# Optimization experiments

Hardware: AMD Instinct MI355X
Metric: run time of the kernel (lower is better)

## Reference

```python
import jax, jax.numpy as jnp
import numpy as np

D_MODEL = 128
REDUCTION = 4
KSIZE = 3
B = D_MODEL  # required by the original code's groups=B conv shape constraint
L = 4096


def setup_inputs() -> dict:
    key = jax.random.key(0)
    ks = jax.random.split(key, 7)
    d, r, K = D_MODEL, REDUCTION, KSIZE
    return {
        "x": jax.random.normal(ks[0], (B, L, d), dtype=jnp.float32),
        "W1": jax.random.normal(ks[1], (d // r, d), dtype=jnp.float32) * (1.0 / np.sqrt(d)),
        "b1": jax.random.normal(ks[2], (d // r,), dtype=jnp.float32) * 0.01,
        "W2": jax.random.normal(ks[3], (K, d // r), dtype=jnp.float32) * (1.0 / np.sqrt(d // r)),
        "b2": jax.random.normal(ks[4], (K,), dtype=jnp.float32) * 0.01,
        "Wc": jax.random.normal(ks[5], (d, d), dtype=jnp.float32) * (1.0 / np.sqrt(d)),
        "bc": jax.random.normal(ks[6], (d,), dtype=jnp.float32) * 0.01,
    }


def reference(x, W1, b1, W2, b2, Wc, bc):
    # x: [B, L, d] with B == d (required by original groups=B conv)
    Bsz, Lseq, d = x.shape
    K = W2.shape[0]
    pad = (K - 1) // 2
    # kernel generation from global average pool
    m = x.mean(axis=1)                                   # [B, d]
    h = jax.nn.gelu(m @ W1.T + b1, approximate=False)    # [B, d//r]
    w = jax.nn.softmax(h @ W2.T + b2, axis=-1)           # [B, K]; row j is the kernel for channel j
    # depthwise-style cross-correlation: y[b, l, c] = sum_k xp[b, l+k, c] * w[c, k]
    xp = jnp.pad(x, ((0, 0), (pad, pad), (0, 0)))        # [B, L+2*pad, d]
    y = sum(xp[:, k:k + Lseq, :] * w[None, None, :, k] for k in range(K))  # [B, L, d]
    # pointwise conv (kernel_size=1) == per-token linear
    return y @ Wc.T + bc                                 # [B, L, d]
```

## Files before the change

kernel.cpp:

```cpp
#include <hip/hip_runtime.h>
#include <hip/hip_bf16.h>

#define D_MODEL 128
#define SEQ_L   4096
#define BATCH   128
#define TM      128
#define NSEG    8

typedef float f4 __attribute__((ext_vector_type(4)));
typedef float f32x4 __attribute__((ext_vector_type(4)));
typedef short bf16x8 __attribute__((ext_vector_type(8)));

__device__ __forceinline__ unsigned short f2bf(float f) {
    union { float f; unsigned u; } v; v.f = f;
    unsigned r = v.u + 0x7FFFu + ((v.u >> 16) & 1u);
    return (unsigned short)(r >> 16);
}

__global__ __launch_bounds__(256) void kmean(const float* __restrict__ x,
                                             float* __restrict__ part) {
    int seg = blockIdx.x, b = blockIdx.y;
    int t = threadIdx.x;
    int c4 = t & 31, ph = t >> 5;
    const f4* xb = reinterpret_cast<const f4*>(x + (size_t)b * SEQ_L * D_MODEL);
    int l0 = seg * (SEQ_L / NSEG);
    f4 acc = {0.f, 0.f, 0.f, 0.f};
    for (int l = l0 + ph; l < l0 + SEQ_L / NSEG; l += 8)
        acc += xb[l * 32 + c4];
    __shared__ f4 red[256];
    red[t] = acc;
    __syncthreads();
    if (t < 32) {
        f4 s = red[t];
        #pragma unroll
        for (int p = 1; p < 8; ++p) s += red[t + 32 * p];
        reinterpret_cast<f4*>(part + ((size_t)b * NSEG + seg) * D_MODEL)[t] = s;
    }
}

__global__ __launch_bounds__(128) void kweights(const float* __restrict__ part,
                                                const float* __restrict__ W1,
                                                const float* __restrict__ b1,
                                                const float* __restrict__ W2,
                                                const float* __restrict__ b2,
                                                float* __restrict__ w) {
    int c = threadIdx.x;
    f4 mv[32];
    #pragma unroll
    for (int d4 = 0; d4 < 32; ++d4) mv[d4] = (f4){0.f, 0.f, 0.f, 0.f};
    for (int s = 0; s < NSEG; ++s) {
        const f4* ps = reinterpret_cast<const f4*>(part + ((size_t)c * NSEG + s) * D_MODEL);
        #pragma unroll
        for (int d4 = 0; d4 < 32; ++d4) mv[d4] += ps[d4];
    }
    #pragma unroll
    for (int d4 = 0; d4 < 32; ++d4) mv[d4] *= (1.0f / (float)SEQ_L);

    float h[32];
    #pragma unroll
    for (int j = 0; j < 32; ++j) {
        const f4* w1r = reinterpret_cast<const f4*>(W1 + j * 128);
        f4 s4 = {0.f, 0.f, 0.f, 0.f};
        #pragma unroll
        for (int d4 = 0; d4 < 32; ++d4) s4 += mv[d4] * w1r[d4];
        float s = s4[0] + s4[1] + s4[2] + s4[3] + b1[j];
        h[j] = 0.5f * s * (1.0f + erff(s * 0.70710678118654752f));
    }
    float lg[3];
    float mx = -1e30f;
    #pragma unroll
    for (int k = 0; k < 3; ++k) {
        float s = b2[k];
        #pragma unroll
        for (int j = 0; j < 32; ++j) s += h[j] * W2[k * 32 + j];
        lg[k] = s;
        mx = fmaxf(mx, s);
    }
    float e[3], den = 0.f;
    #pragma unroll
    for (int k = 0; k < 3; ++k) { e[k] = __expf(lg[k] - mx); den += e[k]; }
    float inv = 1.0f / den;
    #pragma unroll
    for (int k = 0; k < 3; ++k) w[k * 128 + c] = e[k] * inv;
}

__global__ __launch_bounds__(256) void kcvt(const float* __restrict__ Wc,
                                            unsigned short* __restrict__ wcb) {
    int i = blockIdx.x * 256 + threadIdx.x;
    f4 v = reinterpret_cast<const f4*>(Wc)[i];
    ushort4 o;
    o.x = f2bf(v[0]); o.y = f2bf(v[1]); o.z = f2bf(v[2]); o.w = f2bf(v[3]);
    reinterpret_cast<ushort4*>(wcb)[i] = o;
}

__global__ __launch_bounds__(512, 4) void kconv(const float* __restrict__ x,
                                                const float* __restrict__ w,
                                                const unsigned short* __restrict__ wcb,
                                                const float* __restrict__ bc,
                                                float* __restrict__ out) {
    __shared__ __align__(16) unsigned short y_lds[TM][136];
    __shared__ __align__(16) unsigned short wc_lds[128][136];

    int t = threadIdx.x;
    int b = blockIdx.y;
    int l0 = blockIdx.x * TM;
    const float* xb = x + (size_t)b * SEQ_L * D_MODEL;

    int c4 = t & 31;
    f4 w0 = reinterpret_cast<const f4*>(w)[c4];
    f4 w1 = reinterpret_cast<const f4*>(w + 128)[c4];
    f4 w2 = reinterpret_cast<const f4*>(w + 256)[c4];

    {
        int rg = t >> 5;
        int r0 = rg * 8;
        int lb = l0 + r0;
        f4 prev = (lb > 0) ? reinterpret_cast<const f4*>(xb + (size_t)(lb - 1) * D_MODEL)[c4]
                           : (f4){0.f, 0.f, 0.f, 0.f};
        f4 cur = reinterpret_cast<const f4*>(xb + (size_t)lb * D_MODEL)[c4];
        #pragma unroll
        for (int i = 0; i < 8; ++i) {
            int l = lb + i;
            f4 nxt = (l < SEQ_L - 1)
                         ? reinterpret_cast<const f4*>(xb + (size_t)(l + 1) * D_MODEL)[c4]
                         : (f4){0.f, 0.f, 0.f, 0.f};
            f4 y = prev * w0 + cur * w1 + nxt * w2;
            ushort4 yb;
            yb.x = f2bf(y[0]); yb.y = f2bf(y[1]); yb.z = f2bf(y[2]); yb.w = f2bf(y[3]);
            *reinterpret_cast<ushort4*>(&y_lds[r0 + i][c4 * 4]) = yb;
            prev = cur;
            cur = nxt;
        }
    }

    {
        int row = t >> 4;
        int u16 = t & 15;
        #pragma unroll
        for (int p = 0; p < 4; ++p) {
            int rr = row + p * 32;
            uint4 v = reinterpret_cast<const uint4*>(wcb + (size_t)rr * 128)[u16];
            *reinterpret_cast<uint4*>(&wc_lds[rr][u16 * 8]) = v;
        }
    }
    __syncthreads();

    int lane = t & 63, wid = t >> 6;
    int lrow = wid * 16 + (lane & 15);
    int kb = (lane >> 4) * 8;

    f32x4 acc[8];
    #pragma unroll
    for (int n = 0; n < 8; ++n) acc[n] = (f32x4){0.f, 0.f, 0.f, 0.f};

    #pragma unroll
    for (int kc = 0; kc < 4; ++kc) {
        bf16x8 by = *reinterpret_cast<const bf16x8*>(&y_lds[lrow][kc * 32 + kb]);
        #pragma unroll
        for (int n = 0; n < 8; ++n) {
            bf16x8 awc = *reinterpret_cast<const bf16x8*>(&wc_lds[n * 16 + (lane & 15)][kc * 32 + kb]);
            acc[n] = __builtin_amdgcn_mfma_f32_16x16x32_bf16(awc, by, acc[n], 0, 0, 0);
        }
    }

    int l = l0 + wid * 16 + (lane & 15);
    int cb = (lane >> 4) * 4;
    float* orow = out + ((size_t)b * SEQ_L + l) * D_MODEL;
    #pragma unroll
    for (int n = 0; n < 8; ++n) {
        f4 bcv = *reinterpret_cast<const f4*>(bc + n * 16 + cb);
        f4 v = acc[n] + bcv;
        *reinterpret_cast<f4*>(orow + n * 16 + cb) = v;
    }
}

extern "C" void kernel_launch(void* const* d_in, const int* in_sizes, int n_in,
                              void* d_out, int out_size, void* d_ws, size_t ws_size,
                              hipStream_t stream) {
    const float* x  = (const float*)d_in[0];
    const float* W1 = (const float*)d_in[1];
    const float* b1 = (const float*)d_in[2];
    const float* W2 = (const float*)d_in[3];
    const float* b2 = (const float*)d_in[4];
    const float* Wc = (const float*)d_in[5];
    const float* bc = (const float*)d_in[6];
    float* out = (float*)d_out;

    char* ws = (char*)d_ws;
    float* part = (float*)ws;
    float* w    = (float*)(ws + 524288);
    unsigned short* wcb = (unsigned short*)(ws + 526336);

    kmean<<<dim3(NSEG, BATCH), 256, 0, stream>>>(x, part);
    kweights<<<1, 128, 0, stream>>>(part, W1, b1, W2, b2, w);
    kcvt<<<16, 256, 0, stream>>>(Wc, wcb);
    kconv<<<dim3(SEQ_L / TM, BATCH), 512, 0, stream>>>(x, w, wcb, bc, out);
}
```

Baseline: 264.5 us.

## Keep Wc slice in registers per wave and unroll mean reduction

The conv kernel stops staging the bf16 pointwise weight matrix in LDS. Each wave instead loads its own 16 output-channel rows of Wc into registers and loops over 8 token tiles, reading only the y tile from LDS. This cuts the LDS footprint and the per-MFMA LDS reads for weights, at the cost of more scattered output stores. The mean kernel is widened to 512 threads with four independent accumulators to raise memory-level parallelism.

```diff
diff --git a/kernel.cpp b/kernel.cpp
--- a/kernel.cpp
+++ b/kernel.cpp
@@ -6,6 +6,7 @@
 #define BATCH   128
 #define TM      128
 #define NSEG    8
+#define YPAD    132
 
 typedef float f4 __attribute__((ext_vector_type(4)));
 typedef float f32x4 __attribute__((ext_vector_type(4)));
@@ -17,23 +18,31 @@
     return (unsigned short)(r >> 16);
 }
 
-__global__ __launch_bounds__(256) void kmean(const float* __restrict__ x,
+__global__ __launch_bounds__(512) void kmean(const float* __restrict__ x,
                                              float* __restrict__ part) {
     int seg = blockIdx.x, b = blockIdx.y;
     int t = threadIdx.x;
     int c4 = t & 31, ph = t >> 5;
     const f4* xb = reinterpret_cast<const f4*>(x + (size_t)b * SEQ_L * D_MODEL);
     int l0 = seg * (SEQ_L / NSEG);
-    f4 acc = {0.f, 0.f, 0.f, 0.f};
-    for (int l = l0 + ph; l < l0 + SEQ_L / NSEG; l += 8)
-        acc += xb[l * 32 + c4];
-    __shared__ f4 red[256];
+
+    f4 a0 = {0.f,0.f,0.f,0.f}, a1 = a0, a2 = a0, a3 = a0;
+    #pragma unroll
+    for (int i = 0; i < 32; i += 4) {
+        a0 += xb[(l0 + ph + (i + 0) * 16) * 32 + c4];
+        a1 += xb[(l0 + ph + (i + 1) * 16) * 32 + c4];
+        a2 += xb[(l0 + ph + (i + 2) * 16) * 32 + c4];
+        a3 += xb[(l0 + ph + (i + 3) * 16) * 32 + c4];
+    }
+    f4 acc = (a0 + a1) + (a2 + a3);
+
+    __shared__ f4 red[512];
     red[t] = acc;
     __syncthreads();
     if (t < 32) {
         f4 s = red[t];
         #pragma unroll
-        for (int p = 1; p < 8; ++p) s += red[t + 32 * p];
+        for (int p = 1; p < 16; ++p) s += red[t + 32 * p];
         reinterpret_cast<f4*>(part + ((size_t)b * NSEG + seg) * D_MODEL)[t] = s;
     }
 }
@@ -98,13 +107,22 @@
                                                 const unsigned short* __restrict__ wcb,
                                                 const float* __restrict__ bc,
                                                 float* __restrict__ out) {
-    __shared__ __align__(16) unsigned short y_lds[TM][136];
-    __shared__ __align__(16) unsigned short wc_lds[128][136];
+    __shared__ __align__(16) unsigned short y_lds[TM][YPAD];
 
     int t = threadIdx.x;
     int b = blockIdx.y;
     int l0 = blockIdx.x * TM;
     const float* xb = x + (size_t)b * SEQ_L * D_MODEL;
+
+    int lane = t & 63, wid = t >> 6;
+    int co0 = wid * 16;
+    int arow = co0 + (lane & 15);
+    int kb = (lane >> 4) * 8;
+
+    bf16x8 awc[4];
+    #pragma unroll
+    for (int kc = 0; kc < 4; ++kc)
+        awc[kc] = *reinterpret_cast<const bf16x8*>(wcb + (size_t)arow * 128 + kc * 32 + kb);
 
     int c4 = t & 31;
     f4 w0 = reinterpret_cast<const f4*>(w)[c4];
@@ -132,45 +150,28 @@
             cur = nxt;
         }
     }
-
-    {
-        int row = t >> 4;
-        int u16 = t & 15;
-        #pragma unroll
-        for (int p = 0; p < 4; ++p) {
-            int rr = row + p * 32;
-            uint4 v = reinterpret_cast<const uint4*>(wcb + (size_t)rr * 128)[u16];
-            *reinterpret_cast<uint4*>(&wc_lds[rr][u16 * 8]) = v;
-        }
-    }
     __syncthreads();
-
-    int lane = t & 63, wid = t >> 6;
-    int lrow = wid * 16 + (lane & 15);
-    int kb = (lane >> 4) * 8;
 
     f32x4 acc[8];
     #pragma unroll
-    for (int n = 0; n < 8; ++n) acc[n] = (f32x4){0.f, 0.f, 0.f, 0.f};
+    for (int tt = 0; tt < 8; ++tt) acc[tt] = (f32x4){0.f, 0.f, 0.f, 0.f};
 
     #pragma unroll
-    for (int kc = 0; kc < 4; ++kc) {
-        bf16x8 by = *reinterpret_cast<const bf16x8*>(&y_lds[lrow][kc * 32 + kb]);
+    for (int tt = 0; tt < 8; ++tt) {
         #pragma unroll
-        for (int n = 0; n < 8; ++n) {
-            bf16x8 awc = *reinterpret_cast<const bf16x8*>(&wc_lds[n * 16 + (lane & 15)][kc * 32 + kb]);
-            acc[n] = __builtin_amdgcn_mfma_f32_16x16x32_bf16(awc, by, acc[n], 0, 0, 0);
+        for (int kc = 0; kc < 4; ++kc) {
+            bf16x8 by = *reinterpret_cast<const bf16x8*>(&y_lds[tt * 16 + (lane & 15)][kc * 32 + kb]);
+            acc[tt] = __builtin_amdgcn_mfma_f32_16x16x32_bf16(awc[kc], by, acc[tt], 0, 0, 0);
         }
     }
 
-    int l = l0 + wid * 16 + (lane & 15);
     int cb = (lane >> 4) * 4;
-    float* orow = out + ((size_t)b * SEQ_L + l) * D_MODEL;
+    f4 bcv = *reinterpret_cast<const f4*>(bc + co0 + cb);
     #pragma unroll
-    for (int n = 0; n < 8; ++n) {
-        f4 bcv = *reinterpret_cast<const f4*>(bc + n * 16 + cb);
-        f4 v = acc[n] + bcv;
-        *reinterpret_cast<f4*>(orow + n * 16 + cb) = v;
+    for (int tt = 0; tt < 8; ++tt) {
+        int l = l0 + tt * 16 + (lane & 15);
+        f4 v = acc[tt] + bcv;
+        *reinterpret_cast<f4*>(out + ((size_t)b * SEQ_L + l) * D_MODEL + co0 + cb) = v;
     }
 }
 
@@ -191,7 +192,7 @@
     float* w    = (float*)(ws + 524288);
     unsigned short* wcb = (unsigned short*)(ws + 526336);
 
-    kmean<<<dim3(NSEG, BATCH), 256, 0, stream>>>(x, part);
+    kmean<<<dim3(NSEG, BATCH), 512, 0, stream>>>(x, part);
     kweights<<<1, 128, 0, stream>>>(part, W1, b1, W2, b2, w);
     kcvt<<<16, 256, 0, stream>>>(Wc, wcb);
     kconv<<<dim3(SEQ_L / TM, BATCH), 512, 0, stream>>>(x, w, wcb, bc, out);
```

Result: faster. 251.9 us (-4.7%).
